# Performance work log

Hardware: AMD Instinct MI355X
Metric: run time of the kernel (lower is better)

The kernel has to match this reference:

```python
import jax, jax.numpy as jnp
import numpy as np
from jax import lax

T = 8  # hardcoded temporal length in the torch module

def _dwconv_t(z, w, b):
    # z: (N, C, T, 1); w: (C, 1, k, 1) depthwise; 'same' padding along T
    k = w.shape[2]
    p = (k - 1) // 2
    out = lax.conv_general_dilated(
        z, w, window_strides=(1, 1), padding=[(p, p), (0, 0)],
        feature_group_count=z.shape[1],
        dimension_numbers=('NCHW', 'OIHW', 'NCHW'))
    return out + b[None, :, None, None]


def setup_inputs() -> dict:
    key = jax.random.key(0)
    ks = jax.random.split(key, 13)
    C, IC, H, W, B = 1024, 512, 14, 14, 16
    s = lambda k, shp, scale: jax.random.normal(k, shp, dtype=jnp.float32) * scale
    return {
        'x':   s(ks[0], (B * T, C, H, W), 1.0),
        'w1':  s(ks[1], (IC, C, 1, 1), 0.03),
        'b1':  s(ks[2], (IC,), 0.02),
        'wb1': s(ks[3], (IC, 1, 1, 1), 0.3),
        'bb1': s(ks[4], (IC,), 0.02),
        'wb2': s(ks[5], (IC, 1, 3, 1), 0.3),
        'bb2': s(ks[6], (IC,), 0.02),
        'wb3': s(ks[7], (IC, 1, 5, 1), 0.3),
        'bb3': s(ks[8], (IC,), 0.02),
        'wb4': s(ks[9], (IC, 1, 7, 1), 0.3),
        'bb4': s(ks[10], (IC,), 0.02),
        'w2':  s(ks[11], (C, IC, 1, 1), 0.03),
        'b2':  s(ks[12], (C,), 0.02),
    }


def reference(x, w1, b1, wb1, bb1, wb2, bb2, wb3, bb3, wb4, bb4, w2, b2):
    BT, C, H, W = x.shape
    B = BT // T
    IC = w1.shape[0]
    # conv1: 1x1 pointwise conv == channel GEMM
    y = jnp.einsum('nchw,oc->nohw', x, w1[:, :, 0, 0]) + b1[None, :, None, None]
    # (B*T, IC, H, W) -> (B, T, IC, H, W) -> (B, H, W, IC, T) -> (B*H*W, IC, T, 1)
    z = y.reshape(B, T, IC, H, W).transpose(0, 3, 4, 2, 1).reshape(B * H * W, IC, T, 1)
    out = (_dwconv_t(z, wb1, bb1) + _dwconv_t(z, wb2, bb2)
           + _dwconv_t(z, wb3, bb3) + _dwconv_t(z, wb4, bb4))
    # (B*H*W, IC, T, 1) -> (B, H, W, IC, T) -> (B, T, IC, H, W) -> (B*T, IC, H, W)
    out = out.reshape(B, H, W, IC, T).transpose(0, 4, 3, 1, 2).reshape(BT, IC, H, W)
    # conv2: 1x1 pointwise conv back to C channels
    out = jnp.einsum('nihw,oi->nohw', out, w2[:, :, 0, 0]) + b2[None, :, None, None]
    return x + out
```

## Files before the change

kernel.cpp:

```cpp
#include <hip/hip_runtime.h>
#include <hip/hip_bf16.h>

typedef short short8 __attribute__((ext_vector_type(8)));
typedef float f32x4 __attribute__((ext_vector_type(4)));
typedef unsigned int uint;

#define CB   16
#define TT   8
#define CIN  1024
#define ICH  512
#define HWS  196
#define NPB  1568
#define NF   25088

static __device__ __forceinline__ unsigned short f2bf(float f) {
  __hip_bfloat16 h = __float2bfloat16(f); unsigned short u; __builtin_memcpy(&u, &h, 2); return u;
}

static __device__ __forceinline__ void stage16(const void* g, void* l) {
  __builtin_amdgcn_global_load_lds(
      (const __attribute__((address_space(1))) unsigned int*)(unsigned long long)g,
      (__attribute__((address_space(3))) unsigned int*)(unsigned int)(unsigned long long)l,
      16, 0, 0);
}

__global__ void k_prep_w(const float* __restrict__ w1, const float* __restrict__ w2,
    const float* __restrict__ wb1, const float* __restrict__ bb1,
    const float* __restrict__ wb2, const float* __restrict__ bb2,
    const float* __restrict__ wb3, const float* __restrict__ bb3,
    const float* __restrict__ wb4, const float* __restrict__ bb4,
    __hip_bfloat16* __restrict__ w1b, __hip_bfloat16* __restrict__ w2b,
    float* __restrict__ weff, float* __restrict__ beff) {
  int idx = blockIdx.x * 256 + threadIdx.x;
  if (idx < CIN * ICH) {
    w1b[idx] = __float2bfloat16(w1[idx]);
    w2b[idx] = __float2bfloat16(w2[idx]);
  }
  if (idx < ICH) {
    float e[7];
#pragma unroll
    for (int u = 0; u < 7; u++) e[u] = wb4[idx * 7 + u];
#pragma unroll
    for (int u = 0; u < 5; u++) e[u + 1] += wb3[idx * 5 + u];
#pragma unroll
    for (int u = 0; u < 3; u++) e[u + 2] += wb2[idx * 3 + u];
    e[3] += wb1[idx];
#pragma unroll
    for (int u = 0; u < 7; u++) weff[idx * 8 + u] = e[u];
    weff[idx * 8 + 7] = 0.f;
    beff[idx] = bb1[idx] + bb2[idx] + bb3[idx] + bb4[idx];
  }
}

__global__ __launch_bounds__(448) void k_prep_x(const float* __restrict__ x,
                                                __hip_bfloat16* __restrict__ xbT) {
  __shared__ unsigned short tile[196 * 128];
  int xcd = blockIdx.x & 7, i = blockIdx.x >> 3;
  int id = xcd * 128 + i;
  int bt = id >> 3, cr = id & 7;
  int c0 = cr * 128;
  int b = bt >> 3, t = bt & 7;
  const float* src = x + ((size_t)bt * CIN + c0) * HWS;
  int tid = threadIdx.x;
#pragma unroll
  for (int it = 0; it < 14; it++) {
    int idx = it * 448 + tid;
    f32x4 v = *(const f32x4*)(src + (size_t)idx * 4);
    int c = idx / 49, hwq = idx - c * 49;
#pragma unroll
    for (int j = 0; j < 4; j++) {
      int hw = hwq * 4 + j;
      int slot = (c >> 3) ^ ((hw + (hw >> 2)) & 15);
      tile[hw * 128 + slot * 8 + (c & 7)] = f2bf(v[j]);
    }
  }
  __syncthreads();
  __hip_bfloat16* dstb = xbT + ((size_t)b * NPB + (size_t)t) * CIN + c0;
#pragma unroll
  for (int it = 0; it < 7; it++) {
    int idx = it * 448 + tid;
    int hw = idx >> 4, co = idx & 15;
    int slot = co ^ ((hw + (hw >> 2)) & 15);
    uint4 val = *(const uint4*)&tile[hw * 128 + slot * 8];
    *(uint4*)(dstb + (size_t)(hw * 8) * CIN + co * 8) = val;
  }
}

template <int KD>
static __device__ __forceinline__ void gemm_core16(
    const __hip_bfloat16* __restrict__ Ar,
    const __hip_bfloat16* __restrict__ Br,
    __hip_bfloat16* As, __hip_bfloat16* Bs, f32x4 (&acc)[4][4]) {
  constexpr int NT = KD / 64;
  const int tid = threadIdx.x;
  const int lane = tid & 63, w = tid >> 6;
  const int wm = w >> 2, wn = w & 3;
  const int ln = lane & 15, lm = lane >> 4;
  const int srow = lane >> 3;
  const int schk = (lane & 7) ^ srow;
  const __hip_bfloat16* aS = Ar + (size_t)(w * 8 + srow) * KD + schk * 8;
  const __hip_bfloat16* bS = Br + (size_t)(w * 8 + srow) * KD + schk * 8;
  __hip_bfloat16* aD = As + (w * 8) * 64;
  __hip_bfloat16* bD = Bs + (w * 8) * 64;
  const int ck0 = ((lm) ^ (ln & 7)) * 8;
  const int ck1 = ((4 + lm) ^ (ln & 7)) * 8;
  const int rab = (wm * 16 + ln) * 64;
  const int rbb = (wn * 64 + ln) * 64;

#define STG(src, dst, h, kt, buf) \
  stage16(src + (size_t)((h) * 128) * KD + (kt) * 64, dst + (buf) * 16384 + ((h) * 128) * 64)

  STG(bS, bD, 0, 0, 0); STG(bS, bD, 1, 0, 0);
  STG(aS, aD, 0, 0, 0); STG(aS, aD, 1, 0, 0);

  short8 af0, af1, bfA[4], bfB[4];
  for (int t = 0; t < NT; t++) {
    const int buf = t & 1, nb = buf ^ 1;
    const bool has = (t + 1 < NT);
    const __hip_bfloat16* Ab = As + buf * 16384;
    const __hip_bfloat16* Bb = Bs + buf * 16384;
    if (has) STG(bS, bD, 0, t + 1, nb);
    if (has) asm volatile("s_waitcnt vmcnt(2)" ::: "memory");
    else     asm volatile("s_waitcnt vmcnt(1)" ::: "memory");
    asm volatile("s_barrier" ::: "memory");
    af0 = *(const short8*)&Ab[rab + ck0];
    af1 = *(const short8*)&Ab[rab + 4096 + ck0];
#pragma unroll
    for (int nf = 0; nf < 4; nf++) bfA[nf] = *(const short8*)&Bb[rbb + nf * 1024 + ck0];
    asm volatile("s_waitcnt lgkmcnt(0)" ::: "memory");
    __builtin_amdgcn_sched_barrier(0);
    __builtin_amdgcn_s_setprio(1);
#pragma unroll
    for (int nf = 0; nf < 4; nf++) {
      acc[0][nf] = __builtin_amdgcn_mfma_f32_16x16x32_bf16(af0, bfA[nf], acc[0][nf], 0, 0, 0);
      acc[1][nf] = __builtin_amdgcn_mfma_f32_16x16x32_bf16(af1, bfA[nf], acc[1][nf], 0, 0, 0);
    }
    __builtin_amdgcn_s_setprio(0);
    if (has) STG(bS, bD, 1, t + 1, nb);
    af0 = *(const short8*)&Ab[rab + ck1];
    af1 = *(const short8*)&Ab[rab + 4096 + ck1];
#pragma unroll
    for (int nf = 0; nf < 4; nf++) bfB[nf] = *(const short8*)&Bb[rbb + nf * 1024 + ck1];
    asm volatile("s_waitcnt lgkmcnt(0)" ::: "memory");
    __builtin_amdgcn_sched_barrier(0);
    __builtin_amdgcn_s_setprio(1);
#pragma unroll
    for (int nf = 0; nf < 4; nf++) {
      acc[0][nf] = __builtin_amdgcn_mfma_f32_16x16x32_bf16(af0, bfB[nf], acc[0][nf], 0, 0, 0);
      acc[1][nf] = __builtin_amdgcn_mfma_f32_16x16x32_bf16(af1, bfB[nf], acc[1][nf], 0, 0, 0);
    }
    __builtin_amdgcn_s_setprio(0);
    if (has) STG(aS, aD, 0, t + 1, nb);
    if (has) asm volatile("s_waitcnt vmcnt(3)" ::: "memory");
    else     asm volatile("s_waitcnt vmcnt(0)" ::: "memory");
    asm volatile("s_barrier" ::: "memory");
    af0 = *(const short8*)&Ab[rab + 2 * 4096 + ck0];
    af1 = *(const short8*)&Ab[rab + 3 * 4096 + ck0];
    asm volatile("s_waitcnt lgkmcnt(0)" ::: "memory");
    __builtin_amdgcn_sched_barrier(0);
    __builtin_amdgcn_s_setprio(1);
#pragma unroll
    for (int nf = 0; nf < 4; nf++) {
      acc[2][nf] = __builtin_amdgcn_mfma_f32_16x16x32_bf16(af0, bfA[nf], acc[2][nf], 0, 0, 0);
      acc[3][nf] = __builtin_amdgcn_mfma_f32_16x16x32_bf16(af1, bfA[nf], acc[3][nf], 0, 0, 0);
    }
    __builtin_amdgcn_s_setprio(0);
    if (has) STG(aS, aD, 1, t + 1, nb);
    af0 = *(const short8*)&Ab[rab + 2 * 4096 + ck1];
    af1 = *(const short8*)&Ab[rab + 3 * 4096 + ck1];
    asm volatile("s_waitcnt lgkmcnt(0)" ::: "memory");
    __builtin_amdgcn_sched_barrier(0);
    asm volatile("s_barrier" ::: "memory");
    __builtin_amdgcn_s_setprio(1);
#pragma unroll
    for (int nf = 0; nf < 4; nf++) {
      acc[2][nf] = __builtin_amdgcn_mfma_f32_16x16x32_bf16(af0, bfB[nf], acc[2][nf], 0, 0, 0);
      acc[3][nf] = __builtin_amdgcn_mfma_f32_16x16x32_bf16(af1, bfB[nf], acc[3][nf], 0, 0, 0);
    }
    __builtin_amdgcn_s_setprio(0);
  }
#undef STG
}

__global__ __launch_bounds__(1024, 4) void k_gemm1(const __hip_bfloat16* __restrict__ xbT,
                                                   const __hip_bfloat16* __restrict__ w1b,
                                                   const float* __restrict__ b1,
                                                   const float* __restrict__ weff,
                                                   const float* __restrict__ beff,
                                                   __hip_bfloat16* __restrict__ dwT) {
  __shared__ __hip_bfloat16 As[2 * 256 * 64];
  __shared__ __hip_bfloat16 Bs[2 * 256 * 64];
  int xcd = blockIdx.x & 7, i = blockIdx.x >> 3;
  int id = (xcd < 4 ? xcd * 25 : 100 + (xcd - 4) * 24) + i;
  int rt = id >> 1, ot = id & 1;
  int n0 = rt * 256, o0 = ot * 256;
  f32x4 acc[4][4];
#pragma unroll
  for (int a = 0; a < 4; a++)
#pragma unroll
    for (int c = 0; c < 4; c++) acc[a][c] = (f32x4){0.f, 0.f, 0.f, 0.f};
  gemm_core16<1024>(xbT + (size_t)n0 * CIN, w1b + (size_t)o0 * CIN, As, Bs, acc);

  int tid = threadIdx.x, lane = tid & 63, w = tid >> 6;
  int wm = w >> 2, wn = w & 3, ln = lane & 15, lm = lane >> 4;
  bool hiT = (lm & 1);
#pragma unroll
  for (int nf = 0; nf < 4; nf++) {
    int o = o0 + wn * 64 + nf * 16 + ln;
    float e[7];
#pragma unroll
    for (int u = 0; u < 7; u++) e[u] = weff[o * 8 + u];
    float be = beff[o];
    float bo = b1[o];
#pragma unroll
    for (int mf = 0; mf < 4; mf++) {
      float av[4], pv[4];
#pragma unroll
      for (int j = 0; j < 4; j++) av[j] = acc[mf][nf][j] + bo;
#pragma unroll
      for (int j = 0; j < 4; j++) pv[j] = __shfl_xor(av[j], 16, 64);
      float ov[4];
      if (hiT) {
#pragma unroll
        for (int j = 0; j < 4; j++) {
          float s = be;
#pragma unroll
          for (int u = 0; u < 7; u++) {
            int ss = 4 + j + u - 3;
            if (ss >= 0 && ss < 8) s += e[u] * (ss < 4 ? pv[ss] : av[ss - 4]);
          }
          ov[j] = s;
        }
      } else {
#pragma unroll
        for (int j = 0; j < 4; j++) {
          float s = be;
#pragma unroll
          for (int u = 0; u < 7; u++) {
            int ss = j + u - 3;
            if (ss >= 0 && ss < 8) s += e[u] * (ss < 4 ? av[ss] : pv[ss - 4]);
          }
          ov[j] = s;
        }
      }
      int grow = n0 + mf * 64 + wm * 16 + ((lm >> 1) & 1) * 8;
      int gidx = grow >> 3;
      int gb = gidx / HWS, ghw = gidx - gb * HWS;
      int tb = hiT ? 4 : 0;
#pragma unroll
      for (int j = 0; j < 4; j++) {
        size_t rr = (size_t)gb * NPB + (size_t)(tb + j) * HWS + ghw;
        dwT[rr * ICH + o] = __float2bfloat16(ov[j]);
      }
    }
  }
}

__global__ __launch_bounds__(1024, 4) void k_gemm2(const __hip_bfloat16* __restrict__ dwT,
                                                   const __hip_bfloat16* __restrict__ w2b,
                                                   const float* __restrict__ b2,
                                                   const float* __restrict__ xres,
                                                   float* __restrict__ out) {
  __shared__ __align__(16) char smem[131072];
  __hip_bfloat16* As = (__hip_bfloat16*)smem;
  __hip_bfloat16* Bs = (__hip_bfloat16*)(smem + 65536);
  int id = (blockIdx.x & 7) * 49 + (blockIdx.x >> 3);
  int nt = id >> 2, mt = id & 3;
  int n0 = nt * 256, m0 = mt * 256;
  f32x4 acc[4][4];
#pragma unroll
  for (int a = 0; a < 4; a++)
#pragma unroll
    for (int c = 0; c < 4; c++) acc[a][c] = (f32x4){0.f, 0.f, 0.f, 0.f};
  gemm_core16<512>(w2b + (size_t)m0 * ICH, dwT + (size_t)n0 * ICH, As, Bs, acc);

  int tid = threadIdx.x, lane = tid & 63, w = tid >> 6;
  int wm = w >> 2, wn = w & 3, ln = lane & 15, lm = lane >> 4;
  float* arr = (float*)smem;
  int fc = tid & 63, fr = tid >> 6;
  int n2 = n0 + fc * 4;
  int bb = n2 / NPB, r = n2 - bb * NPB;
  int t2 = r / HWS, hw = r - t2 * HWS;
  size_t base4 = ((size_t)((bb * TT + t2) * CIN)) * HWS + hw;
#pragma unroll
  for (int p = 0; p < 4; p++) {
    __syncthreads();
#pragma unroll
    for (int nf = 0; nf < 4; nf++)
#pragma unroll
      for (int j = 0; j < 4; j++)
        arr[(wm * 16 + lm * 4 + j) * 260 + wn * 64 + nf * 16 + ln] = acc[p][nf][j];
    __syncthreads();
#pragma unroll
    for (int it = 0; it < 4; it++) {
      int o2l = it * 16 + fr;
      f32x4 v = *(const f32x4*)&arr[o2l * 260 + fc * 4];
      int o2 = m0 + p * 64 + o2l;
      float bo = b2[o2];
      size_t a = base4 + (size_t)o2 * HWS;
      float4 xr = *(const float4*)(xres + a);
      float4 ov = make_float4(v[0] + bo + xr.x, v[1] + bo + xr.y,
                              v[2] + bo + xr.z, v[3] + bo + xr.w);
      *(float4*)(out + a) = ov;
    }
  }
}

extern "C" void kernel_launch(void* const* d_in, const int* in_sizes, int n_in,
                              void* d_out, int out_size, void* d_ws, size_t ws_size,
                              hipStream_t stream) {
  const float* x   = (const float*)d_in[0];
  const float* w1  = (const float*)d_in[1];
  const float* b1  = (const float*)d_in[2];
  const float* wb1 = (const float*)d_in[3];
  const float* bb1 = (const float*)d_in[4];
  const float* wb2 = (const float*)d_in[5];
  const float* bb2 = (const float*)d_in[6];
  const float* wb3 = (const float*)d_in[7];
  const float* bb3 = (const float*)d_in[8];
  const float* wb4 = (const float*)d_in[9];
  const float* bb4 = (const float*)d_in[10];
  const float* w2  = (const float*)d_in[11];
  const float* b2  = (const float*)d_in[12];
  float* out = (float*)d_out;

  __hip_bfloat16* xbT = (__hip_bfloat16*)d_out;

  char* ws = (char*)d_ws;
  __hip_bfloat16* dwT = (__hip_bfloat16*)ws;
  __hip_bfloat16* w1b = (__hip_bfloat16*)(ws + 25690112);
  __hip_bfloat16* w2b = (__hip_bfloat16*)(ws + 25690112 + 1048576);
  float* weff = (float*)(ws + 25690112 + 2097152);
  float* beff = weff + 4096;

  k_prep_w<<<(CIN * ICH + 255) / 256, 256, 0, stream>>>(
      w1, w2, wb1, bb1, wb2, bb2, wb3, bb3, wb4, bb4, w1b, w2b, weff, beff);
  k_prep_x<<<1024, 448, 0, stream>>>(x, xbT);
  k_gemm1<<<196, 1024, 0, stream>>>(xbT, w1b, b1, weff, beff, dwT);
  k_gemm2<<<392, 1024, 0, stream>>>(dwT, w2b, b2, x, out);
}
```

Measured before the change: 117.3 us.

## Retile both GEMMs to 512-thread blocks with 256x128 tiles and BK=32

New measurement: 124.8 us. +6.4%, slower.

```diff
diff --git a/kernel.cpp b/kernel.cpp
--- a/kernel.cpp
+++ b/kernel.cpp
@@ -87,122 +87,84 @@
 }
 
 template <int KD>
-static __device__ __forceinline__ void gemm_core16(
+static __device__ __forceinline__ void gemm_core8(
     const __hip_bfloat16* __restrict__ Ar,
     const __hip_bfloat16* __restrict__ Br,
     __hip_bfloat16* As, __hip_bfloat16* Bs, f32x4 (&acc)[4][4]) {
-  constexpr int NT = KD / 64;
+  constexpr int NT = KD / 32;
   const int tid = threadIdx.x;
   const int lane = tid & 63, w = tid >> 6;
-  const int wm = w >> 2, wn = w & 3;
+  const int wm = w >> 1, wn = w & 1;
   const int ln = lane & 15, lm = lane >> 4;
-  const int srow = lane >> 3;
-  const int schk = (lane & 7) ^ srow;
-  const __hip_bfloat16* aS = Ar + (size_t)(w * 8 + srow) * KD + schk * 8;
-  const __hip_bfloat16* bS = Br + (size_t)(w * 8 + srow) * KD + schk * 8;
-  __hip_bfloat16* aD = As + (w * 8) * 64;
-  __hip_bfloat16* bD = Bs + (w * 8) * 64;
-  const int ck0 = ((lm) ^ (ln & 7)) * 8;
-  const int ck1 = ((4 + lm) ^ (ln & 7)) * 8;
-  const int rab = (wm * 16 + ln) * 64;
-  const int rbb = (wn * 64 + ln) * 64;
-
-#define STG(src, dst, h, kt, buf) \
-  stage16(src + (size_t)((h) * 128) * KD + (kt) * 64, dst + (buf) * 16384 + ((h) * 128) * 64)
-
-  STG(bS, bD, 0, 0, 0); STG(bS, bD, 1, 0, 0);
-  STG(aS, aD, 0, 0, 0); STG(aS, aD, 1, 0, 0);
-
-  short8 af0, af1, bfA[4], bfB[4];
+  const int srow = lane >> 2;
+  const int schk = (lane & 3) ^ ((lane >> 2) & 3) ^ ((lane >> 4) & 3);
+  const __hip_bfloat16* aS = Ar + (size_t)(w * 16 + srow) * KD + schk * 8;
+  const __hip_bfloat16* bS = Br + (size_t)(w * 16 + srow) * KD + schk * 8;
+  const int ck = (lm ^ (ln & 3) ^ ((ln >> 2) & 3)) * 8;
+  int ra[4], rb[4];
+#pragma unroll
+  for (int mf = 0; mf < 4; mf++) ra[mf] = (wm * 64 + mf * 16 + ln) * 32 + ck;
+#pragma unroll
+  for (int nf = 0; nf < 4; nf++) rb[nf] = (wn * 64 + nf * 16 + ln) * 32 + ck;
+
+#define STGA(h, kt, buf) \
+  stage16(aS + (size_t)((h) * 128) * KD + (kt) * 32, \
+          As + (buf) * 8192 + ((h) * 128 + w * 16) * 32)
+#define STGB(kt, buf) \
+  stage16(bS + (size_t)(kt) * 32, Bs + (buf) * 4096 + (w * 16) * 32)
+
+  STGA(0, 0, 0); STGA(1, 0, 0); STGB(0, 0);
+
+  short8 af[4], bf[4];
   for (int t = 0; t < NT; t++) {
     const int buf = t & 1, nb = buf ^ 1;
     const bool has = (t + 1 < NT);
-    const __hip_bfloat16* Ab = As + buf * 16384;
-    const __hip_bfloat16* Bb = Bs + buf * 16384;
-    if (has) STG(bS, bD, 0, t + 1, nb);
-    if (has) asm volatile("s_waitcnt vmcnt(2)" ::: "memory");
-    else     asm volatile("s_waitcnt vmcnt(1)" ::: "memory");
-    asm volatile("s_barrier" ::: "memory");
-    af0 = *(const short8*)&Ab[rab + ck0];
-    af1 = *(const short8*)&Ab[rab + 4096 + ck0];
-#pragma unroll
-    for (int nf = 0; nf < 4; nf++) bfA[nf] = *(const short8*)&Bb[rbb + nf * 1024 + ck0];
-    asm volatile("s_waitcnt lgkmcnt(0)" ::: "memory");
-    __builtin_amdgcn_sched_barrier(0);
-    __builtin_amdgcn_s_setprio(1);
-#pragma unroll
-    for (int nf = 0; nf < 4; nf++) {
-      acc[0][nf] = __builtin_amdgcn_mfma_f32_16x16x32_bf16(af0, bfA[nf], acc[0][nf], 0, 0, 0);
-      acc[1][nf] = __builtin_amdgcn_mfma_f32_16x16x32_bf16(af1, bfA[nf], acc[1][nf], 0, 0, 0);
-    }
-    __builtin_amdgcn_s_setprio(0);
-    if (has) STG(bS, bD, 1, t + 1, nb);
-    af0 = *(const short8*)&Ab[rab + ck1];
-    af1 = *(const short8*)&Ab[rab + 4096 + ck1];
-#pragma unroll
-    for (int nf = 0; nf < 4; nf++) bfB[nf] = *(const short8*)&Bb[rbb + nf * 1024 + ck1];
-    asm volatile("s_waitcnt lgkmcnt(0)" ::: "memory");
-    __builtin_amdgcn_sched_barrier(0);
-    __builtin_amdgcn_s_setprio(1);
-#pragma unroll
-    for (int nf = 0; nf < 4; nf++) {
-      acc[0][nf] = __builtin_amdgcn_mfma_f32_16x16x32_bf16(af0, bfB[nf], acc[0][nf], 0, 0, 0);
-      acc[1][nf] = __builtin_amdgcn_mfma_f32_16x16x32_bf16(af1, bfB[nf], acc[1][nf], 0, 0, 0);
-    }
-    __builtin_amdgcn_s_setprio(0);
-    if (has) STG(aS, aD, 0, t + 1, nb);
+    const __hip_bfloat16* Ab = As + buf * 8192;
+    const __hip_bfloat16* Bb = Bs + buf * 4096;
+    if (has) { STGA(0, t + 1, nb); STGA(1, t + 1, nb); STGB(t + 1, nb); }
     if (has) asm volatile("s_waitcnt vmcnt(3)" ::: "memory");
     else     asm volatile("s_waitcnt vmcnt(0)" ::: "memory");
     asm volatile("s_barrier" ::: "memory");
-    af0 = *(const short8*)&Ab[rab + 2 * 4096 + ck0];
-    af1 = *(const short8*)&Ab[rab + 3 * 4096 + ck0];
-    asm volatile("s_waitcnt lgkmcnt(0)" ::: "memory");
-    __builtin_amdgcn_sched_barrier(0);
-    __builtin_amdgcn_s_setprio(1);
-#pragma unroll
-    for (int nf = 0; nf < 4; nf++) {
-      acc[2][nf] = __builtin_amdgcn_mfma_f32_16x16x32_bf16(af0, bfA[nf], acc[2][nf], 0, 0, 0);
-      acc[3][nf] = __builtin_amdgcn_mfma_f32_16x16x32_bf16(af1, bfA[nf], acc[3][nf], 0, 0, 0);
-    }
-    __builtin_amdgcn_s_setprio(0);
-    if (has) STG(aS, aD, 1, t + 1, nb);
-    af0 = *(const short8*)&Ab[rab + 2 * 4096 + ck1];
-    af1 = *(const short8*)&Ab[rab + 3 * 4096 + ck1];
+#pragma unroll
+    for (int mf = 0; mf < 4; mf++) af[mf] = *(const short8*)&Ab[ra[mf]];
+#pragma unroll
+    for (int nf = 0; nf < 4; nf++) bf[nf] = *(const short8*)&Bb[rb[nf]];
     asm volatile("s_waitcnt lgkmcnt(0)" ::: "memory");
     __builtin_amdgcn_sched_barrier(0);
     asm volatile("s_barrier" ::: "memory");
     __builtin_amdgcn_s_setprio(1);
 #pragma unroll
-    for (int nf = 0; nf < 4; nf++) {
-      acc[2][nf] = __builtin_amdgcn_mfma_f32_16x16x32_bf16(af0, bfB[nf], acc[2][nf], 0, 0, 0);
-      acc[3][nf] = __builtin_amdgcn_mfma_f32_16x16x32_bf16(af1, bfB[nf], acc[3][nf], 0, 0, 0);
-    }
+    for (int nf = 0; nf < 4; nf++)
+#pragma unroll
+      for (int mf = 0; mf < 4; mf++)
+        acc[mf][nf] = __builtin_amdgcn_mfma_f32_16x16x32_bf16(af[mf], bf[nf], acc[mf][nf], 0, 0, 0);
     __builtin_amdgcn_s_setprio(0);
   }
-#undef STG
-}
-
-__global__ __launch_bounds__(1024, 4) void k_gemm1(const __hip_bfloat16* __restrict__ xbT,
-                                                   const __hip_bfloat16* __restrict__ w1b,
-                                                   const float* __restrict__ b1,
-                                                   const float* __restrict__ weff,
-                                                   const float* __restrict__ beff,
-                                                   __hip_bfloat16* __restrict__ dwT) {
-  __shared__ __hip_bfloat16 As[2 * 256 * 64];
-  __shared__ __hip_bfloat16 Bs[2 * 256 * 64];
+#undef STGA
+#undef STGB
+}
+
+__global__ __launch_bounds__(512, 4) void k_gemm1(const __hip_bfloat16* __restrict__ xbT,
+                                                  const __hip_bfloat16* __restrict__ w1b,
+                                                  const float* __restrict__ b1,
+                                                  const float* __restrict__ weff,
+                                                  const float* __restrict__ beff,
+                                                  __hip_bfloat16* __restrict__ dwT) {
+  __shared__ __hip_bfloat16 As[2 * 256 * 32];
+  __shared__ __hip_bfloat16 Bs[2 * 128 * 32];
   int xcd = blockIdx.x & 7, i = blockIdx.x >> 3;
-  int id = (xcd < 4 ? xcd * 25 : 100 + (xcd - 4) * 24) + i;
-  int rt = id >> 1, ot = id & 1;
-  int n0 = rt * 256, o0 = ot * 256;
+  int id = xcd * 49 + i;
+  int nt = id >> 2, ot = id & 3;
+  int n0 = nt * 256, o0 = ot * 128;
   f32x4 acc[4][4];
 #pragma unroll
   for (int a = 0; a < 4; a++)
 #pragma unroll
     for (int c = 0; c < 4; c++) acc[a][c] = (f32x4){0.f, 0.f, 0.f, 0.f};
-  gemm_core16<1024>(xbT + (size_t)n0 * CIN, w1b + (size_t)o0 * CIN, As, Bs, acc);
+  gemm_core8<1024>(xbT + (size_t)n0 * CIN, w1b + (size_t)o0 * CIN, As, Bs, acc);
 
   int tid = threadIdx.x, lane = tid & 63, w = tid >> 6;
-  int wm = w >> 2, wn = w & 3, ln = lane & 15, lm = lane >> 4;
+  int wm = w >> 1, wn = w & 1, ln = lane & 15, lm = lane >> 4;
   bool hiT = (lm & 1);
 #pragma unroll
   for (int nf = 0; nf < 4; nf++) {
@@ -243,7 +205,7 @@
           ov[j] = s;
         }
       }
-      int grow = n0 + mf * 64 + wm * 16 + ((lm >> 1) & 1) * 8;
+      int grow = n0 + wm * 64 + mf * 16 + ((lm >> 1) & 1) * 8;
       int gidx = grow >> 3;
       int gb = gidx / HWS, ghw = gidx - gb * HWS;
       int tb = hiT ? 4 : 0;
@@ -256,28 +218,29 @@
   }
 }
 
-__global__ __launch_bounds__(1024, 4) void k_gemm2(const __hip_bfloat16* __restrict__ dwT,
-                                                   const __hip_bfloat16* __restrict__ w2b,
-                                                   const float* __restrict__ b2,
-                                                   const float* __restrict__ xres,
-                                                   float* __restrict__ out) {
-  __shared__ __align__(16) char smem[131072];
+__global__ __launch_bounds__(512, 4) void k_gemm2(const __hip_bfloat16* __restrict__ dwT,
+                                                  const __hip_bfloat16* __restrict__ w2b,
+                                                  const float* __restrict__ b2,
+                                                  const float* __restrict__ xres,
+                                                  float* __restrict__ out) {
+  __shared__ __align__(16) char smem[49152];
   __hip_bfloat16* As = (__hip_bfloat16*)smem;
-  __hip_bfloat16* Bs = (__hip_bfloat16*)(smem + 65536);
-  int id = (blockIdx.x & 7) * 49 + (blockIdx.x >> 3);
+  __hip_bfloat16* Bs = (__hip_bfloat16*)(smem + 32768);
+  int xcd = blockIdx.x & 7, i = blockIdx.x >> 3;
+  int id = xcd * 98 + i;
   int nt = id >> 2, mt = id & 3;
-  int n0 = nt * 256, m0 = mt * 256;
+  int n0 = nt * 128, m0 = mt * 256;
   f32x4 acc[4][4];
 #pragma unroll
   for (int a = 0; a < 4; a++)
 #pragma unroll
     for (int c = 0; c < 4; c++) acc[a][c] = (f32x4){0.f, 0.f, 0.f, 0.f};
-  gemm_core16<512>(w2b + (size_t)m0 * ICH, dwT + (size_t)n0 * ICH, As, Bs, acc);
+  gemm_core8<512>(w2b + (size_t)m0 * ICH, dwT + (size_t)n0 * ICH, As, Bs, acc);
 
   int tid = threadIdx.x, lane = tid & 63, w = tid >> 6;
-  int wm = w >> 2, wn = w & 3, ln = lane & 15, lm = lane >> 4;
+  int wm = w >> 1, wn = w & 1, ln = lane & 15, lm = lane >> 4;
   float* arr = (float*)smem;
-  int fc = tid & 63, fr = tid >> 6;
+  int fc = tid & 31, fr = tid >> 5;
   int n2 = n0 + fc * 4;
   int bb = n2 / NPB, r = n2 - bb * NPB;
   int t2 = r / HWS, hw = r - t2 * HWS;
@@ -285,16 +248,20 @@
 #pragma unroll
   for (int p = 0; p < 4; p++) {
     __syncthreads();
-#pragma unroll
-    for (int nf = 0; nf < 4; nf++)
-#pragma unroll
-      for (int j = 0; j < 4; j++)
-        arr[(wm * 16 + lm * 4 + j) * 260 + wn * 64 + nf * 16 + ln] = acc[p][nf][j];
+    if (wm == p) {
+#pragma unroll
+      for (int nf = 0; nf < 4; nf++)
+#pragma unroll
+        for (int mf = 0; mf < 4; mf++)
+#pragma unroll
+          for (int j = 0; j < 4; j++)
+            arr[(mf * 16 + lm * 4 + j) * 132 + wn * 64 + nf * 16 + ln] = acc[mf][nf][j];
+    }
     __syncthreads();
 #pragma unroll
     for (int it = 0; it < 4; it++) {
       int o2l = it * 16 + fr;
-      f32x4 v = *(const f32x4*)&arr[o2l * 260 + fc * 4];
+      f32x4 v = *(const f32x4*)&arr[o2l * 132 + fc * 4];
       int o2 = m0 + p * 64 + o2l;
       float bo = b2[o2];
       size_t a = base4 + (size_t)o2 * HWS;
@@ -336,6 +303,6 @@
   k_prep_w<<<(CIN * ICH + 255) / 256, 256, 0, stream>>>(
       w1, w2, wb1, bb1, wb2, bb2, wb3, bb3, wb4, bb4, w1b, w2b, weff, beff);
   k_prep_x<<<1024, 448, 0, stream>>>(x, xbT);
-  k_gemm1<<<196, 1024, 0, stream>>>(xbT, w1b, b1, weff, beff, dwT);
-  k_gemm2<<<392, 1024, 0, stream>>>(dwT, w2b, b2, x, out);
-}
+  k_gemm1<<<392, 512, 0, stream>>>(xbT, w1b, b1, weff, beff, dwT);
+  k_gemm2<<<784, 512, 0, stream>>>(dwT, w2b, b2, x, out);
+}
```
